# Optimization experiments

Hardware: AMD Instinct MI355X
Metric: run time of the kernel (lower is better)

The kernel has to match this reference:

```python
import jax, jax.numpy as jnp
import numpy as np

N_TRANSFORMS = 24
N_INIT = 5
SOFT_BLEND = 5.0
MAX_STEPS = 8   # reduced from 50 for reference runtime; same per-step math
CVG = 1e-5
DVG = 1.0
EPS = 1e-6


def posi_enc(x):
    # min_deg=0, max_deg=4, append_identity: [...,3] -> [...,27]
    scales = jnp.asarray([1.0, 2.0, 4.0, 8.0], x.dtype)
    xb = (x[..., None, :] * scales[:, None]).reshape(x.shape[:-1] + (12,))
    return jnp.concatenate([x, jnp.sin(xb), jnp.cos(xb)], axis=-1)


def mlp(h, params):
    for W, b in params[:-1]:
        h = jax.nn.relu(h @ W + b)
    W, b = params[-1]
    return h @ W + b


def setup_inputs() -> dict:
    key = jax.random.key(0)
    ks = jax.random.split(key, 16)
    B, N, J = 1, 32768, N_TRANSFORMS
    x = jax.random.normal(ks[0], (B, N, 3), jnp.float32)
    bone_pts = jax.random.normal(ks[1], (J, 3), jnp.float32)

    def near_id(k):
        A = jnp.eye(4, dtype=jnp.float32) + 0.05 * jax.random.normal(k, (J, 4, 4), jnp.float32)
        return A.at[:, 3, :].set(jnp.asarray([0.0, 0.0, 0.0, 1.0], jnp.float32))

    inp = dict(
        x=x, bone_pts=bone_pts,
        transforms=near_id(ks[2]), delta_transforms=near_id(ks[3]),
        W0=0.1 * jax.random.normal(ks[4], (27, 128), jnp.float32), b0=jnp.zeros((128,), jnp.float32),
        W1=0.1 * jax.random.normal(ks[5], (128, 128), jnp.float32), b1=jnp.zeros((128,), jnp.float32),
        W2=0.1 * jax.random.normal(ks[6], (128, 128), jnp.float32), b2=jnp.zeros((128,), jnp.float32),
        W3=0.1 * jax.random.normal(ks[7], (128, 128), jnp.float32), b3=jnp.zeros((128,), jnp.float32),
        W4=0.1 * jax.random.normal(ks[8], (128, 25), jnp.float32), b4=jnp.zeros((25,), jnp.float32),
    )
    return inp


def reference(x, bone_pts, transforms, delta_transforms, W0, b0, W1, b1, W2, b2, W3, b3, W4, b4):
    params = [(W0, b0), (W1, b1), (W2, b2), (W3, b3), (W4, b4)]
    B, N, _ = x.shape
    I = N_INIT + 1  # with_bkgd appends identity init
    dt = x.dtype

    # ---- _initialize_canonical: KNN over bone distances, gather delta transforms
    d = jnp.linalg.norm(x[:, :, None, :] - bone_pts, axis=-1)          # [B,N,J]
    idx = jax.lax.top_k(-d, N_INIT)[1]                                  # [B,N,5]
    Tsel = delta_transforms[idx]                                        # [B,N,5,4,4]
    eye4 = jnp.broadcast_to(jnp.eye(4, dtype=dt), (B, N, 1, 4, 4))
    Tinit = jnp.concatenate([Tsel, eye4], axis=2)                       # [B,N,I,4,4]
    xh = jnp.concatenate([x, jnp.ones_like(x[..., :1])], axis=-1)
    xc0 = jnp.einsum('bnipq,bnq->bnip', Tinit[..., :3, :4], xh)         # [B,N,I,3]

    M = B * N * I
    target = jnp.broadcast_to(x[:, :, None, :], (B, N, I, 3)).reshape(M, 3)
    x0 = xc0.reshape(M, 3)
    Tfull = jnp.concatenate([transforms, jnp.eye(4, dtype=dt)[None]], axis=0)  # [J+1,4,4]

    def g(xc):  # forward-skinning residual g(x_cano) = LBS(x_cano) - x_world
        w = jax.nn.softmax(SOFT_BLEND * mlp(posi_enc(xc), params), axis=-1)   # [M,25]
        tf = jnp.einsum('mj,jpq->mpq', w, Tfull)                               # [M,4,4]
        return jnp.einsum('mpq,mq->mp', tf[:, :3, :3], xc) + tf[:, :3, 3] - target

    # ---- Broyden with dense per-point masking (replaces torch boolean indexing)
    Jinv0 = jnp.broadcast_to(jnp.eye(3, dtype=dt), (M, 3, 3))
    gx0 = g(x0)
    upd0 = -(Jinv0 @ gx0[:, :, None])[:, :, 0]
    norm0 = jnp.linalg.norm(gx0, axis=-1)
    zeros3 = jnp.zeros((M, 3), dt)
    state = (x0, gx0, Jinv0, upd0, x0, norm0, zeros3, zeros3, jnp.ones((M,), bool))

    def body(_, s):
        xk, gx, Jinv, upd, xopt, nopt, dx, dgx, mask = s
        m3 = mask[:, None]
        dx = jnp.where(m3, upd, dx)
        xk = jnp.where(m3, xk + dx, xk)
        gnew = g(xk)
        dgx = jnp.where(m3, gnew - gx, dgx)
        gx = jnp.where(m3, gx + dgx, gx)
        gn = jnp.linalg.norm(gx, axis=-1)
        better = gn < nopt
        nopt = jnp.where(better, gn, nopt)
        xopt = jnp.where(better[:, None], xk, xopt)
        mask = (nopt > CVG) & (gn < DVG)
        vT = dx[:, None, :] @ Jinv                                      # [M,1,3]
        a = dx[:, :, None] - Jinv @ dgx[:, :, None]                      # [M,3,1]
        b = vT @ dgx[:, :, None]                                         # [M,1,1]
        b = b + jnp.where(b >= 0, EPS, -EPS)
        Jinv = jnp.where(mask[:, None, None], Jinv + (a / b) @ vT, Jinv)
        upd = jnp.where(m3, -(Jinv @ gx[:, :, None])[:, :, 0], upd)
        return (xk, gx, Jinv, upd, xopt, nopt, dx, dgx, mask)

    state = jax.lax.fori_loop(0, MAX_STEPS, body, state)
    xopt, nopt = state[4], state[5]
    xopt = jax.lax.stop_gradient(xopt)  # torch detaches the root solve
    valid = nopt < CVG

    # differentiable final forward skinning at the found canonical points
    w = jax.nn.softmax(SOFT_BLEND * mlp(posi_enc(xopt), params), axis=-1)
    tf = jnp.einsum('mj,jpq->mpq', w, Tfull)
    xw = jnp.einsum('mpq,mq->mp', tf[:, :3, :3], xopt) + tf[:, :3, 3]

    return (xw.reshape(B, N, I, 3), xopt.reshape(B, N, I, 3),
            nopt.reshape(B, N, I), valid.reshape(B, N, I))
```

## Files before the change

### kernel.cpp

```cpp
#include <hip/hip_runtime.h>
#include <math.h>

#define BLOCK 256
#define PPB 64
#define HP 132
#define WCOLS 2136
#define NTILES 56

typedef float v2f __attribute__((ext_vector_type(2)));

__device__ __forceinline__ v2f mkv2(float a, float b) {
    v2f r; r.x = a; r.y = b; return r;
}
__device__ __forceinline__ v2f pkfma(v2f a, v2f b, v2f c) {
#if __has_builtin(__builtin_elementwise_fma)
    return __builtin_elementwise_fma(a, b, c);
#else
    return mkv2(fmaf(a.x, b.x, c.x), fmaf(a.y, b.y, c.y));
#endif
}
__device__ __forceinline__ float f4el(const float4& v, int r) {
    return (r == 0) ? v.x : (r == 1) ? v.y : (r == 2) ? v.z : v.w;
}
__device__ __forceinline__ int col_base(int p) { return p * HP + ((p >> 2) << 3); }

__global__ void prep_kernel(const float* __restrict__ W0, const float* __restrict__ W1,
                            const float* __restrict__ W2, const float* __restrict__ W3,
                            const float* __restrict__ W4, const float* __restrict__ b4,
                            float* __restrict__ Wt, float* __restrict__ b4p) {
    const int d = blockIdx.x * blockDim.x + threadIdx.x;
    if (d < NTILES * 1024) {
        const int t = d >> 10, w = d & 1023;
        float v;
        if (t < 52) {
            const int r = w >> 7, rem = w & 127;
            const int half = rem >> 6, q = (rem >> 2) & 15, jl = rem & 3;
            const int col = q * 8 + half * 4 + jl;
            if (t < 4)       { const int k = t * 8 + r;        v = (k < 27) ? W0[k * 128 + col] : 0.f; }
            else if (t < 20) { const int k = (t - 4) * 8 + r;  v = W1[k * 128 + col]; }
            else if (t < 36) { const int k = (t - 20) * 8 + r; v = W2[k * 128 + col]; }
            else             { const int k = (t - 36) * 8 + r; v = W3[k * 128 + col]; }
        } else {
            const int r = w >> 5, rem = w & 31;
            const int half = (rem >> 4) & 1, s = (rem >> 2) & 3, jl = rem & 3;
            const int col = s * 8 + half * 4 + jl;
            const int k = (t - 52) * 32 + r;
            v = (col < 25) ? W4[k * 25 + col] : 0.f;
        }
        Wt[d] = v;
    }
    if (d < 32) b4p[d] = (d < 25) ? b4[d] : 0.f;
}

__device__ __forceinline__ void batch4(const float* wt, int r0, int cg,
                                       const float* hg, int k0,
                                       v2f* __restrict__ acc) {
    float4 h4[4];
#pragma unroll
    for (int p = 0; p < 4; ++p) h4[p] = *(const float4*)(hg + p * HP + k0);
    float4 w0[4], w1[4];
#pragma unroll
    for (int r = 0; r < 4; ++r) {
        w0[r] = *(const float4*)(wt + (r0 + r) * 128 + cg * 4);
        w1[r] = *(const float4*)(wt + (r0 + r) * 128 + 64 + cg * 4);
    }
#pragma unroll
    for (int r = 0; r < 4; ++r) {
        const v2f wa = mkv2(w0[r].x, w0[r].y), wb2 = mkv2(w0[r].z, w0[r].w);
        const v2f wc = mkv2(w1[r].x, w1[r].y), wd = mkv2(w1[r].z, w1[r].w);
#pragma unroll
        for (int p = 0; p < 4; ++p) {
            const float hv = f4el(h4[p], r);
            const v2f hh = mkv2(hv, hv);
            acc[p * 4 + 0] = pkfma(hh, wa, acc[p * 4 + 0]);
            acc[p * 4 + 1] = pkfma(hh, wb2, acc[p * 4 + 1]);
            acc[p * 4 + 2] = pkfma(hh, wc, acc[p * 4 + 2]);
            acc[p * 4 + 3] = pkfma(hh, wd, acc[p * 4 + 3]);
        }
    }
}

__global__ __launch_bounds__(BLOCK)
__attribute__((amdgpu_num_vgpr(128))) void snarf_kernel(
    const float* __restrict__ xin, const float* __restrict__ bone_pts,
    const float* __restrict__ transforms, const float* __restrict__ delta_tf,
    const float* __restrict__ Wt, const float* __restrict__ b0,
    const float* __restrict__ b1, const float* __restrict__ b2,
    const float* __restrict__ b3, const float* __restrict__ b4p,
    float* __restrict__ out, int Npts) {
    __shared__ float hL[4 * WCOLS];
    __shared__ float stL[25 * PPB];
    __shared__ float wb[2][1024];
    __shared__ int flags[4];
    const int tid = threadIdx.x;
    const int wid = tid >> 6;
    const int lane = tid & 63;
    const int p16 = lane & 15;
    const int sq = lane >> 4;
    const int cg = lane >> 2;
    const int gg = lane & 3;
    const int M = Npts * 6;
    const int m = blockIdx.x * PPB + wid * 16 + p16;
    const int mc = (m < M) ? m : (M - 1);
    const int n = mc / 6;
    const int i = mc - n * 6;

    float* hWv = &hL[wid * WCOLS];
    const float* hg = hWv + gg * 536;
    float* hwr = hWv + gg * 536 + 8 * cg;
    float* hq = hWv + col_base(p16);
    volatile float* st = &stL[wid * 16 + p16];
#define STS(idx) st[(idx) * PPB]

    const float tx = xin[n * 3 + 0], ty = xin[n * 3 + 1], tz = xin[n * 3 + 2];

    float xk0, xk1, xk2;
    if (i < 5) {
        float dprev = -1.0f;
        int jprev = -1;
        for (int r = 0; r <= i; ++r) {
            float bd = 3.4028235e38f;
            int bj = 0;
            for (int j = 0; j < 24; ++j) {
                const float ax = tx - bone_pts[j * 3 + 0];
                const float ay = ty - bone_pts[j * 3 + 1];
                const float az = tz - bone_pts[j * 3 + 2];
                const float d = sqrtf(ax * ax + ay * ay + az * az);
                const bool taken = (d < dprev) || (d == dprev && j <= jprev);
                if (!taken && d < bd) { bd = d; bj = j; }
            }
            dprev = bd;
            jprev = bj;
        }
        const float* T = delta_tf + jprev * 16;
        xk0 = fmaf(T[0], tx, fmaf(T[1], ty, fmaf(T[2], tz, T[3])));
        xk1 = fmaf(T[4], tx, fmaf(T[5], ty, fmaf(T[6], tz, T[7])));
        xk2 = fmaf(T[8], tx, fmaf(T[9], ty, fmaf(T[10], tz, T[11])));
    } else {
        xk0 = tx; xk1 = ty; xk2 = tz;
    }

    float gx0 = 0.f, gx1 = 0.f, gx2 = 0.f;
    bool mask = (m < M);

    int cur = 0;
    *(float4*)(&wb[0][0] + tid * 4) = *(const float4*)(Wt + tid * 4);
    __syncthreads();

    for (int step = -1; step < 8; ++step) {
        bool m3 = mask;
        if (step >= 0) {
            __syncthreads();
            if ((flags[0] | flags[1] | flags[2] | flags[3]) == 0) break;
            if (m3) {
                const float u0 = STS(9), u1 = STS(10), u2 = STS(11);
                STS(12) = u0; STS(13) = u1; STS(14) = u2;
                xk0 += u0; xk1 += u1; xk2 += u2;
            }
        }
        const float cx0 = xk0, cx1 = xk1, cx2 = xk2;

        {
            const float f = (float)(1 << sq);
            float sx, cxv, sy, cyv, sz, czv;
            sincosf(f * cx0, &sx, &cxv);
            sincosf(f * cx1, &sy, &cyv);
            sincosf(f * cx2, &sz, &czv);
            if (sq == 0) { hq[0] = cx0; hq[1] = cx1; hq[2] = cx2; }
            const int sb = 3 + sq * 3;
            hq[sb + 0] = sx;  hq[sb + 1] = sy;  hq[sb + 2] = sz;
            hq[sb + 12] = cxv; hq[sb + 13] = cyv; hq[sb + 14] = czv;
            if (sq == 3) {
                hq[27] = 0.f; hq[28] = 0.f; hq[29] = 0.f; hq[30] = 0.f; hq[31] = 0.f;
            }
        }

        __builtin_amdgcn_s_setprio(1);
#pragma unroll 1
        for (int L = 0; L < 4; ++L) {
            const int tbase = (L == 0) ? 0 : (4 + (L - 1) * 16);
            const int NT = (L == 0) ? 4 : 16;
            const float* bc = ((L == 0) ? b0 : (L == 1) ? b1 : (L == 2) ? b2 : b3) + 8 * cg;
            v2f acc[16];
            {
                const float4 b0v = *(const float4*)(bc);
                const float4 b1v = *(const float4*)(bc + 4);
#pragma unroll
                for (int p = 0; p < 4; ++p) {
                    acc[p * 4 + 0] = mkv2(b0v.x, b0v.y);
                    acc[p * 4 + 1] = mkv2(b0v.z, b0v.w);
                    acc[p * 4 + 2] = mkv2(b1v.x, b1v.y);
                    acc[p * 4 + 3] = mkv2(b1v.z, b1v.w);
                }
            }
#pragma unroll 1
            for (int t = 0; t < NT; ++t) {
                const float4 stg = *(const float4*)(Wt + (tbase + t + 1) * 1024 + tid * 4);
                batch4(&wb[cur][0], 0, cg, hg, t * 8, acc);
                batch4(&wb[cur][0], 4, cg, hg, t * 8 + 4, acc);
                *(float4*)(&wb[cur ^ 1][0] + tid * 4) = stg;
                __syncthreads();
                cur ^= 1;
            }
#pragma unroll
            for (int p = 0; p < 4; ++p) {
                float4 o0, o1;
                o0.x = fmaxf(acc[p * 4 + 0].x, 0.f); o0.y = fmaxf(acc[p * 4 + 0].y, 0.f);
                o0.z = fmaxf(acc[p * 4 + 1].x, 0.f); o0.w = fmaxf(acc[p * 4 + 1].y, 0.f);
                o1.x = fmaxf(acc[p * 4 + 2].x, 0.f); o1.y = fmaxf(acc[p * 4 + 2].y, 0.f);
                o1.z = fmaxf(acc[p * 4 + 3].x, 0.f); o1.w = fmaxf(acc[p * 4 + 3].y, 0.f);
                *(float4*)(hwr + p * HP) = o0;
                *(float4*)(hwr + p * HP + 4) = o1;
            }
        }

        {
            v2f la[4];
            const float4 bb0 = *(const float4*)(b4p + 8 * sq);
            const float4 bb1 = *(const float4*)(b4p + 8 * sq + 4);
            la[0] = mkv2(bb0.x, bb0.y); la[1] = mkv2(bb0.z, bb0.w);
            la[2] = mkv2(bb1.x, bb1.y); la[3] = mkv2(bb1.z, bb1.w);
#pragma unroll 1
            for (int t = 0; t < 4; ++t) {
                const int nt = (t < 3) ? (53 + t) : 0;
                const float4 stg = *(const float4*)(Wt + nt * 1024 + tid * 4);
                const float* wt = &wb[cur][0];
#pragma unroll 2
                for (int kb = 0; kb < 8; ++kb) {
                    const float4 h4 = *(const float4*)(hq + t * 32 + kb * 4);
#pragma unroll
                    for (int r = 0; r < 4; ++r) {
                        const float4 w0 = *(const float4*)(wt + (kb * 4 + r) * 32 + sq * 4);
                        const float4 w1 = *(const float4*)(wt + (kb * 4 + r) * 32 + 16 + sq * 4);
                        const float hv = f4el(h4, r);
                        const v2f hh = mkv2(hv, hv);
                        la[0] = pkfma(hh, mkv2(w0.x, w0.y), la[0]);
                        la[1] = pkfma(hh, mkv2(w0.z, w0.w), la[1]);
                        la[2] = pkfma(hh, mkv2(w1.x, w1.y), la[2]);
                        la[3] = pkfma(hh, mkv2(w1.z, w1.w), la[3]);
                    }
                }
                *(float4*)(&wb[cur ^ 1][0] + tid * 4) = stg;
                __syncthreads();
                cur ^= 1;
            }
            __builtin_amdgcn_s_setprio(0);
            float4 o0, o1;
            o0.x = la[0].x; o0.y = la[0].y; o0.z = la[1].x; o0.w = la[1].y;
            o1.x = la[2].x; o1.y = la[2].y; o1.z = la[3].x; o1.w = la[3].y;
            *(float4*)(hq + 8 * sq) = o0;
            *(float4*)(hq + 8 * sq + 4) = o1;
        }

        float l25[25];
        {
            const float4 r0 = *(const float4*)(hq + 0);
            const float4 r1 = *(const float4*)(hq + 4);
            const float4 r2 = *(const float4*)(hq + 8);
            const float4 r3 = *(const float4*)(hq + 12);
            const float4 r4 = *(const float4*)(hq + 16);
            const float4 r5 = *(const float4*)(hq + 20);
            l25[0] = r0.x; l25[1] = r0.y; l25[2] = r0.z; l25[3] = r0.w;
            l25[4] = r1.x; l25[5] = r1.y; l25[6] = r1.z; l25[7] = r1.w;
            l25[8] = r2.x; l25[9] = r2.y; l25[10] = r2.z; l25[11] = r2.w;
            l25[12] = r3.x; l25[13] = r3.y; l25[14] = r3.z; l25[15] = r3.w;
            l25[16] = r4.x; l25[17] = r4.y; l25[18] = r4.z; l25[19] = r4.w;
            l25[20] = r5.x; l25[21] = r5.y; l25[22] = r5.z; l25[23] = r5.w;
            l25[24] = hq[24];
        }

        float zm = -3.4028235e38f;
#pragma unroll
        for (int j = 0; j < 25; ++j) {
            l25[j] = 5.0f * l25[j];
            zm = fmaxf(zm, l25[j]);
        }
        float ssum = 0.f;
#pragma unroll
        for (int j = 0; j < 25; ++j) {
            l25[j] = expf(l25[j] - zm);
            ssum += l25[j];
        }
        const float inv = 1.0f / ssum;

        float tf[12];
#pragma unroll
        for (int r = 0; r < 12; ++r) tf[r] = 0.f;
#pragma unroll
        for (int j = 0; j < 24; ++j) {
            const float wj = l25[j] * inv;
            const float* T = transforms + j * 16;
#pragma unroll
            for (int r = 0; r < 12; ++r) tf[r] = fmaf(wj, T[r], tf[r]);
        }
        {
            const float wj = l25[24] * inv;
            tf[0] += wj; tf[5] += wj; tf[10] += wj;
        }
        const float r0 = fmaf(tf[0], cx0, fmaf(tf[1], cx1, fmaf(tf[2], cx2, tf[3])));
        const float r1 = fmaf(tf[4], cx0, fmaf(tf[5], cx1, fmaf(tf[6], cx2, tf[7])));
        const float r2 = fmaf(tf[8], cx0, fmaf(tf[9], cx1, fmaf(tf[10], cx2, tf[11])));

        const float g0 = r0 - tx, g1 = r1 - ty, g2 = r2 - tz;

        if (step == -1) {
            gx0 = g0; gx1 = g1; gx2 = g2;
            const float gn = sqrtf(g0 * g0 + g1 * g1 + g2 * g2);
            STS(21) = gn;
            STS(9) = -g0; STS(10) = -g1; STS(11) = -g2;
            STS(18) = xk0; STS(19) = xk1; STS(20) = xk2;
            STS(22) = r0; STS(23) = r1; STS(24) = r2;
            STS(12) = 0.f; STS(13) = 0.f; STS(14) = 0.f;
            STS(15) = 0.f; STS(16) = 0.f; STS(17) = 0.f;
            STS(0) = 1.f; STS(1) = 0.f; STS(2) = 0.f;
            STS(3) = 0.f; STS(4) = 1.f; STS(5) = 0.f;
            STS(6) = 0.f; STS(7) = 0.f; STS(8) = 1.f;
        } else {
            float J00 = STS(0), J01 = STS(1), J02 = STS(2);
            float J10 = STS(3), J11 = STS(4), J12 = STS(5);
            float J20 = STS(6), J21 = STS(7), J22 = STS(8);
            const float dx0 = STS(12), dx1 = STS(13), dx2 = STS(14);
            float dg0 = STS(15), dg1 = STS(16), dg2 = STS(17);
            float nopt = STS(21);
            if (m3) {
                dg0 = g0 - gx0; dg1 = g1 - gx1; dg2 = g2 - gx2;
                gx0 += dg0; gx1 += dg1; gx2 += dg2;
                STS(15) = dg0; STS(16) = dg1; STS(17) = dg2;
            }
            const float gn = sqrtf(gx0 * gx0 + gx1 * gx1 + gx2 * gx2);
            const bool better = gn < nopt;
            if (better) {
                nopt = gn;
                STS(21) = gn;
                STS(18) = xk0; STS(19) = xk1; STS(20) = xk2;
                STS(22) = r0; STS(23) = r1; STS(24) = r2;
            }
            mask = (nopt > 1e-5f) && (gn < 1.0f) && (m < M);

            const float v0 = dx0 * J00 + dx1 * J10 + dx2 * J20;
            const float v1 = dx0 * J01 + dx1 * J11 + dx2 * J21;
            const float v2 = dx0 * J02 + dx1 * J12 + dx2 * J22;
            const float Jd0 = J00 * dg0 + J01 * dg1 + J02 * dg2;
            const float Jd1 = J10 * dg0 + J11 * dg1 + J12 * dg2;
            const float Jd2 = J20 * dg0 + J21 * dg1 + J22 * dg2;
            const float a0 = dx0 - Jd0, a1 = dx1 - Jd1, a2 = dx2 - Jd2;
            float bden = v0 * dg0 + v1 * dg1 + v2 * dg2;
            bden += (bden >= 0.f) ? 1e-6f : -1e-6f;
            if (mask) {
                const float q0 = a0 / bden, q1 = a1 / bden, q2 = a2 / bden;
                J00 = fmaf(q0, v0, J00); J01 = fmaf(q0, v1, J01); J02 = fmaf(q0, v2, J02);
                J10 = fmaf(q1, v0, J10); J11 = fmaf(q1, v1, J11); J12 = fmaf(q1, v2, J12);
                J20 = fmaf(q2, v0, J20); J21 = fmaf(q2, v1, J21); J22 = fmaf(q2, v2, J22);
                STS(0) = J00; STS(1) = J01; STS(2) = J02;
                STS(3) = J10; STS(4) = J11; STS(5) = J12;
                STS(6) = J20; STS(7) = J21; STS(8) = J22;
            }
            if (m3) {
                STS(9) = -(J00 * gx0 + J01 * gx1 + J02 * gx2);
                STS(10) = -(J10 * gx0 + J11 * gx1 + J12 * gx2);
                STS(11) = -(J20 * gx0 + J21 * gx1 + J22 * gx2);
            }
        }
        {
            const unsigned long long b = __ballot(mask);
            if (lane == 0) flags[wid] = (b != 0ull) ? 1 : 0;
        }
    }

    if (sq == 0 && m < M) {
        const float nopt = STS(21);
        out[(size_t)m * 3 + 0] = STS(22);
        out[(size_t)m * 3 + 1] = STS(23);
        out[(size_t)m * 3 + 2] = STS(24);
        float* xopt_out = out + (size_t)M * 3;
        xopt_out[(size_t)m * 3 + 0] = STS(18);
        xopt_out[(size_t)m * 3 + 1] = STS(19);
        xopt_out[(size_t)m * 3 + 2] = STS(20);
        out[(size_t)M * 6 + m] = nopt;
        out[(size_t)M * 7 + m] = (nopt < 1e-5f) ? 1.0f : 0.0f;
    }
#undef STS
}

extern "C" void kernel_launch(void* const* d_in, const int* in_sizes, int n_in,
                              void* d_out, int out_size, void* d_ws, size_t ws_size,
                              hipStream_t stream) {
    const float* x = (const float*)d_in[0];
    const float* bone_pts = (const float*)d_in[1];
    const float* transforms = (const float*)d_in[2];
    const float* delta_tf = (const float*)d_in[3];
    const float* W0 = (const float*)d_in[4];
    const float* b0 = (const float*)d_in[5];
    const float* W1 = (const float*)d_in[6];
    const float* b1 = (const float*)d_in[7];
    const float* W2 = (const float*)d_in[8];
    const float* b2 = (const float*)d_in[9];
    const float* W3 = (const float*)d_in[10];
    const float* b3 = (const float*)d_in[11];
    const float* W4 = (const float*)d_in[12];
    const float* b4 = (const float*)d_in[13];
    float* out = (float*)d_out;

    float* Wt = (float*)d_ws;
    float* b4p = Wt + NTILES * 1024;

    prep_kernel<<<(NTILES * 1024 + 255) / 256, 256, 0, stream>>>(
        W0, W1, W2, W3, W4, b4, Wt, b4p);

    const int Npts = in_sizes[0] / 3;
    const int M = Npts * 6;
    const int blocks = (M + PPB - 1) / PPB;
    snarf_kernel<<<blocks, BLOCK, 0, stream>>>(
        x, bone_pts, transforms, delta_tf, Wt, b0, b1, b2, b3, b4p, out, Npts);
}
```

Before: 1.747 ms.

## Use single-wave blocks with async global-to-LDS weight staging and no block barriers

Blocks shrink from four waves covering 64 points to one wave covering 32 points. Each lane now accumulates an 8-point by 8-column tile, which doubles the reuse of each weight read from LDS. Weight tiles are double-buffered with global_load_lds and a vmcnt wait instead of register staging plus __syncthreads, and the convergence check becomes a wave ballot. The intent is to remove block-wide barriers and register round-trips for weight staging. The cost is a larger accumulator register footprint under the 128-VGPR cap and a different LDS and occupancy balance.

```diff
diff --git a/kernel.cpp b/kernel.cpp
--- a/kernel.cpp
+++ b/kernel.cpp
@@ -1,10 +1,9 @@
 #include <hip/hip_runtime.h>
 #include <math.h>
-
-#define BLOCK 256
-#define PPB 64
-#define HP 132
-#define WCOLS 2136
+#include <stdint.h>
+
+#define BLOCK 64
+#define PPW 32
 #define NTILES 56
 
 typedef float v2f __attribute__((ext_vector_type(2)));
@@ -22,7 +21,26 @@
 __device__ __forceinline__ float f4el(const float4& v, int r) {
     return (r == 0) ? v.x : (r == 1) ? v.y : (r == 2) ? v.z : v.w;
 }
-__device__ __forceinline__ int col_base(int p) { return p * HP + ((p >> 2) << 3); }
+
+#define VMWAIT() asm volatile("s_waitcnt vmcnt(0)" ::: "memory")
+
+__device__ __forceinline__ void stage_tile(const float* __restrict__ Wt, int t,
+                                           float* dst, int lane) {
+    const float* src = Wt + t * 1024 + lane * 4;
+    float* d0 = dst + lane * 4;
+    __builtin_amdgcn_global_load_lds(
+        (const __attribute__((address_space(1))) uint32_t*)src,
+        (__attribute__((address_space(3))) uint32_t*)d0, 16, 0, 0);
+    __builtin_amdgcn_global_load_lds(
+        (const __attribute__((address_space(1))) uint32_t*)(src + 256),
+        (__attribute__((address_space(3))) uint32_t*)(d0 + 256), 16, 0, 0);
+    __builtin_amdgcn_global_load_lds(
+        (const __attribute__((address_space(1))) uint32_t*)(src + 512),
+        (__attribute__((address_space(3))) uint32_t*)(d0 + 512), 16, 0, 0);
+    __builtin_amdgcn_global_load_lds(
+        (const __attribute__((address_space(1))) uint32_t*)(src + 768),
+        (__attribute__((address_space(3))) uint32_t*)(d0 + 768), 16, 0, 0);
+}
 
 __global__ void prep_kernel(const float* __restrict__ W0, const float* __restrict__ W1,
                             const float* __restrict__ W2, const float* __restrict__ W3,
@@ -41,42 +59,82 @@
             else if (t < 36) { const int k = (t - 20) * 8 + r; v = W2[k * 128 + col]; }
             else             { const int k = (t - 36) * 8 + r; v = W3[k * 128 + col]; }
         } else {
-            const int r = w >> 5, rem = w & 31;
-            const int half = (rem >> 4) & 1, s = (rem >> 2) & 3, jl = rem & 3;
-            const int col = s * 8 + half * 4 + jl;
+            const int r = w >> 5, c = w & 31;
             const int k = (t - 52) * 32 + r;
-            v = (col < 25) ? W4[k * 25 + col] : 0.f;
+            v = (c < 25) ? W4[k * 25 + c] : 0.f;
         }
         Wt[d] = v;
     }
     if (d < 32) b4p[d] = (d < 25) ? b4[d] : 0.f;
 }
 
-__device__ __forceinline__ void batch4(const float* wt, int r0, int cg,
-                                       const float* hg, int k0,
+__device__ __forceinline__ void batch2(const float* wt, int kt, int cg,
+                                       const float* hgg, int kh,
                                        v2f* __restrict__ acc) {
-    float4 h4[4];
-#pragma unroll
-    for (int p = 0; p < 4; ++p) h4[p] = *(const float4*)(hg + p * HP + k0);
-    float4 w0[4], w1[4];
-#pragma unroll
-    for (int r = 0; r < 4; ++r) {
-        w0[r] = *(const float4*)(wt + (r0 + r) * 128 + cg * 4);
-        w1[r] = *(const float4*)(wt + (r0 + r) * 128 + 64 + cg * 4);
-    }
-#pragma unroll
-    for (int r = 0; r < 4; ++r) {
-        const v2f wa = mkv2(w0[r].x, w0[r].y), wb2 = mkv2(w0[r].z, w0[r].w);
-        const v2f wc = mkv2(w1[r].x, w1[r].y), wd = mkv2(w1[r].z, w1[r].w);
-#pragma unroll
-        for (int p = 0; p < 4; ++p) {
-            const float hv = f4el(h4[p], r);
-            const v2f hh = mkv2(hv, hv);
-            acc[p * 4 + 0] = pkfma(hh, wa, acc[p * 4 + 0]);
-            acc[p * 4 + 1] = pkfma(hh, wb2, acc[p * 4 + 1]);
-            acc[p * 4 + 2] = pkfma(hh, wc, acc[p * 4 + 2]);
-            acc[p * 4 + 3] = pkfma(hh, wd, acc[p * 4 + 3]);
-        }
+    const float4 w00 = *(const float4*)(wt + kt * 128 + cg * 4);
+    const float4 w01 = *(const float4*)(wt + kt * 128 + 64 + cg * 4);
+    const float4 w10 = *(const float4*)(wt + (kt + 1) * 128 + cg * 4);
+    const float4 w11 = *(const float4*)(wt + (kt + 1) * 128 + 64 + cg * 4);
+    v2f h[8];
+#pragma unroll
+    for (int j = 0; j < 8; ++j) h[j] = *(const v2f*)(hgg + j * 132 + kh);
+    const v2f a0 = mkv2(w00.x, w00.y), a1 = mkv2(w00.z, w00.w);
+    const v2f a2 = mkv2(w01.x, w01.y), a3 = mkv2(w01.z, w01.w);
+    const v2f b0v = mkv2(w10.x, w10.y), b1v = mkv2(w10.z, w10.w);
+    const v2f b2v = mkv2(w11.x, w11.y), b3v = mkv2(w11.z, w11.w);
+#pragma unroll
+    for (int j = 0; j < 8; ++j) {
+        v2f hh = mkv2(h[j].x, h[j].x);
+        acc[j * 4 + 0] = pkfma(hh, a0, acc[j * 4 + 0]);
+        acc[j * 4 + 1] = pkfma(hh, a1, acc[j * 4 + 1]);
+        acc[j * 4 + 2] = pkfma(hh, a2, acc[j * 4 + 2]);
+        acc[j * 4 + 3] = pkfma(hh, a3, acc[j * 4 + 3]);
+        hh = mkv2(h[j].y, h[j].y);
+        acc[j * 4 + 0] = pkfma(hh, b0v, acc[j * 4 + 0]);
+        acc[j * 4 + 1] = pkfma(hh, b1v, acc[j * 4 + 1]);
+        acc[j * 4 + 2] = pkfma(hh, b2v, acc[j * 4 + 2]);
+        acc[j * 4 + 3] = pkfma(hh, b3v, acc[j * 4 + 3]);
+    }
+}
+
+template <int NT>
+__device__ __forceinline__ void main_layer(const float* __restrict__ Wt,
+                                           const float* __restrict__ bL,
+                                           float (*wb)[1024], int& cur, int& gt,
+                                           const float* hgg, float* hwr,
+                                           int cg, int lane) {
+    v2f acc[32];
+    {
+        const float4 bb0 = *(const float4*)(bL + 8 * cg);
+        const float4 bb1 = *(const float4*)(bL + 8 * cg + 4);
+#pragma unroll
+        for (int j = 0; j < 8; ++j) {
+            acc[j * 4 + 0] = mkv2(bb0.x, bb0.y);
+            acc[j * 4 + 1] = mkv2(bb0.z, bb0.w);
+            acc[j * 4 + 2] = mkv2(bb1.x, bb1.y);
+            acc[j * 4 + 3] = mkv2(bb1.z, bb1.w);
+        }
+    }
+#pragma unroll 1
+    for (int t = 0; t < NT; ++t) {
+        VMWAIT();
+        stage_tile(Wt, (gt == 55) ? 0 : (gt + 1), &wb[cur ^ 1][0], lane);
+        const float* wt = &wb[cur][0];
+#pragma unroll
+        for (int b = 0; b < 4; ++b)
+            batch2(wt, b * 2, cg, hgg, t * 8 + b * 2, acc);
+        cur ^= 1;
+        ++gt;
+    }
+#pragma unroll
+    for (int j = 0; j < 8; ++j) {
+        float4 o0, o1;
+        o0.x = fmaxf(acc[j * 4 + 0].x, 0.f); o0.y = fmaxf(acc[j * 4 + 0].y, 0.f);
+        o0.z = fmaxf(acc[j * 4 + 1].x, 0.f); o0.w = fmaxf(acc[j * 4 + 1].y, 0.f);
+        o1.x = fmaxf(acc[j * 4 + 2].x, 0.f); o1.y = fmaxf(acc[j * 4 + 2].y, 0.f);
+        o1.z = fmaxf(acc[j * 4 + 3].x, 0.f); o1.w = fmaxf(acc[j * 4 + 3].y, 0.f);
+        *(float4*)(hwr + j * 132) = o0;
+        *(float4*)(hwr + j * 132 + 4) = o1;
     }
 }
 
@@ -88,29 +146,28 @@
     const float* __restrict__ b1, const float* __restrict__ b2,
     const float* __restrict__ b3, const float* __restrict__ b4p,
     float* __restrict__ out, int Npts) {
-    __shared__ float hL[4 * WCOLS];
-    __shared__ float stL[25 * PPB];
+    __shared__ float hL[4248];
+    __shared__ float stL[25 * PPW];
     __shared__ float wb[2][1024];
-    __shared__ int flags[4];
-    const int tid = threadIdx.x;
-    const int wid = tid >> 6;
-    const int lane = tid & 63;
-    const int p16 = lane & 15;
-    const int sq = lane >> 4;
+    const int lane = threadIdx.x;
     const int cg = lane >> 2;
     const int gg = lane & 3;
+    const int p32 = lane & 31;
+    const int du = lane >> 5;
     const int M = Npts * 6;
-    const int m = blockIdx.x * PPB + wid * 16 + p16;
+    const int m = blockIdx.x * PPW + p32;
     const int mc = (m < M) ? m : (M - 1);
     const int n = mc / 6;
     const int i = mc - n * 6;
 
-    float* hWv = &hL[wid * WCOLS];
-    const float* hg = hWv + gg * 536;
-    float* hwr = hWv + gg * 536 + 8 * cg;
-    float* hq = hWv + col_base(p16);
-    volatile float* st = &stL[wid * 16 + p16];
-#define STS(idx) st[(idx) * PPB]
+    float* hq = hL + p32 * 132 + ((p32 >> 3) << 3);
+    const float* hgg = hL + gg * 1064;
+    float* hwr = hL + gg * 1064 + 8 * cg;
+    volatile float* st = &stL[p32];
+#define STS(idx) st[(idx) * PPW]
+
+    stage_tile(Wt, 0, &wb[0][0], lane);
+    int cur = 0;
 
     const float tx = xin[n * 3 + 0], ty = xin[n * 3 + 1], tz = xin[n * 3 + 2];
 
@@ -143,15 +200,10 @@
     float gx0 = 0.f, gx1 = 0.f, gx2 = 0.f;
     bool mask = (m < M);
 
-    int cur = 0;
-    *(float4*)(&wb[0][0] + tid * 4) = *(const float4*)(Wt + tid * 4);
-    __syncthreads();
-
     for (int step = -1; step < 8; ++step) {
         bool m3 = mask;
         if (step >= 0) {
-            __syncthreads();
-            if ((flags[0] | flags[1] | flags[2] | flags[3]) == 0) break;
+            if (__ballot(mask) == 0ull) break;
             if (m3) {
                 const float u0 = STS(9), u1 = STS(10), u2 = STS(11);
                 STS(12) = u0; STS(13) = u1; STS(14) = u2;
@@ -161,95 +213,86 @@
         const float cx0 = xk0, cx1 = xk1, cx2 = xk2;
 
         {
-            const float f = (float)(1 << sq);
-            float sx, cxv, sy, cyv, sz, czv;
-            sincosf(f * cx0, &sx, &cxv);
-            sincosf(f * cx1, &sy, &cyv);
-            sincosf(f * cx2, &sz, &czv);
-            if (sq == 0) { hq[0] = cx0; hq[1] = cx1; hq[2] = cx2; }
-            const int sb = 3 + sq * 3;
-            hq[sb + 0] = sx;  hq[sb + 1] = sy;  hq[sb + 2] = sz;
-            hq[sb + 12] = cxv; hq[sb + 13] = cyv; hq[sb + 14] = czv;
-            if (sq == 3) {
+            const float fa = du ? 4.f : 1.f;
+            float sax, cax, say, cay, saz, caz;
+            float sbx, cbx, sby, cby, sbz, cbz;
+            sincosf(fa * cx0, &sax, &cax);
+            sincosf(fa * cx1, &say, &cay);
+            sincosf(fa * cx2, &saz, &caz);
+            sincosf(2.f * fa * cx0, &sbx, &cbx);
+            sincosf(2.f * fa * cx1, &sby, &cby);
+            sincosf(2.f * fa * cx2, &sbz, &cbz);
+            const int sa = 3 + du * 6;
+            hq[sa + 0] = sax; hq[sa + 1] = say; hq[sa + 2] = saz;
+            hq[sa + 3] = sbx; hq[sa + 4] = sby; hq[sa + 5] = sbz;
+            hq[sa + 12] = cax; hq[sa + 13] = cay; hq[sa + 14] = caz;
+            hq[sa + 15] = cbx; hq[sa + 16] = cby; hq[sa + 17] = cbz;
+            if (du == 0) {
+                hq[0] = cx0; hq[1] = cx1; hq[2] = cx2;
+            } else {
                 hq[27] = 0.f; hq[28] = 0.f; hq[29] = 0.f; hq[30] = 0.f; hq[31] = 0.f;
             }
         }
 
         __builtin_amdgcn_s_setprio(1);
-#pragma unroll 1
-        for (int L = 0; L < 4; ++L) {
-            const int tbase = (L == 0) ? 0 : (4 + (L - 1) * 16);
-            const int NT = (L == 0) ? 4 : 16;
-            const float* bc = ((L == 0) ? b0 : (L == 1) ? b1 : (L == 2) ? b2 : b3) + 8 * cg;
-            v2f acc[16];
+        int gt = 0;
+        main_layer<4>(Wt, b0, wb, cur, gt, hgg, hwr, cg, lane);
+        main_layer<16>(Wt, b1, wb, cur, gt, hgg, hwr, cg, lane);
+        main_layer<16>(Wt, b2, wb, cur, gt, hgg, hwr, cg, lane);
+        main_layer<16>(Wt, b3, wb, cur, gt, hgg, hwr, cg, lane);
+
+        {
+            v2f la[8];
             {
-                const float4 b0v = *(const float4*)(bc);
-                const float4 b1v = *(const float4*)(bc + 4);
-#pragma unroll
-                for (int p = 0; p < 4; ++p) {
-                    acc[p * 4 + 0] = mkv2(b0v.x, b0v.y);
-                    acc[p * 4 + 1] = mkv2(b0v.z, b0v.w);
-                    acc[p * 4 + 2] = mkv2(b1v.x, b1v.y);
-                    acc[p * 4 + 3] = mkv2(b1v.z, b1v.w);
-                }
-            }
-#pragma unroll 1
-            for (int t = 0; t < NT; ++t) {
-                const float4 stg = *(const float4*)(Wt + (tbase + t + 1) * 1024 + tid * 4);
-                batch4(&wb[cur][0], 0, cg, hg, t * 8, acc);
-                batch4(&wb[cur][0], 4, cg, hg, t * 8 + 4, acc);
-                *(float4*)(&wb[cur ^ 1][0] + tid * 4) = stg;
-                __syncthreads();
-                cur ^= 1;
-            }
-#pragma unroll
-            for (int p = 0; p < 4; ++p) {
-                float4 o0, o1;
-                o0.x = fmaxf(acc[p * 4 + 0].x, 0.f); o0.y = fmaxf(acc[p * 4 + 0].y, 0.f);
-                o0.z = fmaxf(acc[p * 4 + 1].x, 0.f); o0.w = fmaxf(acc[p * 4 + 1].y, 0.f);
-                o1.x = fmaxf(acc[p * 4 + 2].x, 0.f); o1.y = fmaxf(acc[p * 4 + 2].y, 0.f);
-                o1.z = fmaxf(acc[p * 4 + 3].x, 0.f); o1.w = fmaxf(acc[p * 4 + 3].y, 0.f);
-                *(float4*)(hwr + p * HP) = o0;
-                *(float4*)(hwr + p * HP + 4) = o1;
-            }
-        }
-
-        {
-            v2f la[4];
-            const float4 bb0 = *(const float4*)(b4p + 8 * sq);
-            const float4 bb1 = *(const float4*)(b4p + 8 * sq + 4);
-            la[0] = mkv2(bb0.x, bb0.y); la[1] = mkv2(bb0.z, bb0.w);
-            la[2] = mkv2(bb1.x, bb1.y); la[3] = mkv2(bb1.z, bb1.w);
+                const float* bc = b4p + du * 16;
+                const float4 bb0 = *(const float4*)(bc);
+                const float4 bb1 = *(const float4*)(bc + 4);
+                const float4 bb2 = *(const float4*)(bc + 8);
+                const float4 bb3 = *(const float4*)(bc + 12);
+                la[0] = mkv2(bb0.x, bb0.y); la[1] = mkv2(bb0.z, bb0.w);
+                la[2] = mkv2(bb1.x, bb1.y); la[3] = mkv2(bb1.z, bb1.w);
+                la[4] = mkv2(bb2.x, bb2.y); la[5] = mkv2(bb2.z, bb2.w);
+                la[6] = mkv2(bb3.x, bb3.y); la[7] = mkv2(bb3.z, bb3.w);
+            }
 #pragma unroll 1
             for (int t = 0; t < 4; ++t) {
-                const int nt = (t < 3) ? (53 + t) : 0;
-                const float4 stg = *(const float4*)(Wt + nt * 1024 + tid * 4);
+                VMWAIT();
+                stage_tile(Wt, (t < 3) ? (53 + t) : 0, &wb[cur ^ 1][0], lane);
                 const float* wt = &wb[cur][0];
 #pragma unroll 2
                 for (int kb = 0; kb < 8; ++kb) {
                     const float4 h4 = *(const float4*)(hq + t * 32 + kb * 4);
 #pragma unroll
                     for (int r = 0; r < 4; ++r) {
-                        const float4 w0 = *(const float4*)(wt + (kb * 4 + r) * 32 + sq * 4);
-                        const float4 w1 = *(const float4*)(wt + (kb * 4 + r) * 32 + 16 + sq * 4);
+                        const float* wr = wt + (kb * 4 + r) * 32 + du * 16;
+                        const float4 w0 = *(const float4*)(wr);
+                        const float4 w1 = *(const float4*)(wr + 4);
+                        const float4 w2 = *(const float4*)(wr + 8);
+                        const float4 w3 = *(const float4*)(wr + 12);
                         const float hv = f4el(h4, r);
                         const v2f hh = mkv2(hv, hv);
                         la[0] = pkfma(hh, mkv2(w0.x, w0.y), la[0]);
                         la[1] = pkfma(hh, mkv2(w0.z, w0.w), la[1]);
                         la[2] = pkfma(hh, mkv2(w1.x, w1.y), la[2]);
                         la[3] = pkfma(hh, mkv2(w1.z, w1.w), la[3]);
+                        la[4] = pkfma(hh, mkv2(w2.x, w2.y), la[4]);
+                        la[5] = pkfma(hh, mkv2(w2.z, w2.w), la[5]);
+                        la[6] = pkfma(hh, mkv2(w3.x, w3.y), la[6]);
+                        la[7] = pkfma(hh, mkv2(w3.z, w3.w), la[7]);
                     }
                 }
-                *(float4*)(&wb[cur ^ 1][0] + tid * 4) = stg;
-                __syncthreads();
                 cur ^= 1;
             }
             __builtin_amdgcn_s_setprio(0);
-            float4 o0, o1;
+            float4 o0, o1, o2, o3;
             o0.x = la[0].x; o0.y = la[0].y; o0.z = la[1].x; o0.w = la[1].y;
             o1.x = la[2].x; o1.y = la[2].y; o1.z = la[3].x; o1.w = la[3].y;
-            *(float4*)(hq + 8 * sq) = o0;
-            *(float4*)(hq + 8 * sq + 4) = o1;
+            o2.x = la[4].x; o2.y = la[4].y; o2.z = la[5].x; o2.w = la[5].y;
+            o3.x = la[6].x; o3.y = la[6].y; o3.z = la[7].x; o3.w = la[7].y;
+            *(float4*)(hq + du * 16 + 0) = o0;
+            *(float4*)(hq + du * 16 + 4) = o1;
+            *(float4*)(hq + du * 16 + 8) = o2;
+            *(float4*)(hq + du * 16 + 12) = o3;
         }
 
         float l25[25];
@@ -361,13 +404,9 @@
                 STS(11) = -(J20 * gx0 + J21 * gx1 + J22 * gx2);
             }
         }
-        {
-            const unsigned long long b = __ballot(mask);
-            if (lane == 0) flags[wid] = (b != 0ull) ? 1 : 0;
-        }
-    }
-
-    if (sq == 0 && m < M) {
+    }
+
+    if (du == 0 && m < M) {
         const float nopt = STS(21);
         out[(size_t)m * 3 + 0] = STS(22);
         out[(size_t)m * 3 + 1] = STS(23);
@@ -409,7 +448,7 @@
 
     const int Npts = in_sizes[0] / 3;
     const int M = Npts * 6;
-    const int blocks = (M + PPB - 1) / PPB;
+    const int blocks = (M + PPW - 1) / PPW;
     snarf_kernel<<<blocks, BLOCK, 0, stream>>>(
         x, bone_pts, transforms, delta_tf, Wt, b0, b1, b2, b3, b4p, out, Npts);
 }
```

After: 1.965 ms. 12.5% more time.

## Triple-buffer weight tiles with direct global-to-LDS async loads

Applied to the files above, without the earlier changes.

Replaces the register-staged double-buffered weight tile copy with a three-stage ring that loads global memory straight into LDS via global_load_lds. Each tile iteration waits on vmcnt(1) and then a barrier before issuing the load two tiles ahead, so the fetch overlaps the FMA work and the VGPR round trip plus trailing syncthreads are gone. It costs another 4 KB of LDS, and correctness rests on the hand-written waitcnt/barrier ordering and the tile-index wraparound across steps.

```diff
diff --git a/kernel.cpp b/kernel.cpp
--- a/kernel.cpp
+++ b/kernel.cpp
@@ -1,5 +1,6 @@
 #include <hip/hip_runtime.h>
 #include <math.h>
+#include <stdint.h>
 
 #define BLOCK 256
 #define PPB 64
@@ -23,6 +24,13 @@
     return (r == 0) ? v.x : (r == 1) ? v.y : (r == 2) ? v.z : v.w;
 }
 __device__ __forceinline__ int col_base(int p) { return p * HP + ((p >> 2) << 3); }
+
+__device__ __forceinline__ void stage1(const float* __restrict__ Wt, int t,
+                                       float* dst, int tid) {
+    __builtin_amdgcn_global_load_lds(
+        (const __attribute__((address_space(1))) uint32_t*)(Wt + t * 1024 + tid * 4),
+        (__attribute__((address_space(3))) uint32_t*)(dst + tid * 4), 16, 0, 0);
+}
 
 __global__ void prep_kernel(const float* __restrict__ W0, const float* __restrict__ W1,
                             const float* __restrict__ W2, const float* __restrict__ W3,
@@ -80,6 +88,13 @@
     }
 }
 
+#define TILE_SYNC()                                          \
+    do {                                                     \
+        asm volatile("s_waitcnt vmcnt(1)" ::: "memory");     \
+        __builtin_amdgcn_s_barrier();                        \
+        __builtin_amdgcn_sched_barrier(0);                   \
+    } while (0)
+
 __global__ __launch_bounds__(BLOCK)
 __attribute__((amdgpu_num_vgpr(128))) void snarf_kernel(
     const float* __restrict__ xin, const float* __restrict__ bone_pts,
@@ -90,7 +105,7 @@
     float* __restrict__ out, int Npts) {
     __shared__ float hL[4 * WCOLS];
     __shared__ float stL[25 * PPB];
-    __shared__ float wb[2][1024];
+    __shared__ float wb[3][1024];
     __shared__ int flags[4];
     const int tid = threadIdx.x;
     const int wid = tid >> 6;
@@ -111,6 +126,10 @@
     float* hq = hWv + col_base(p16);
     volatile float* st = &stL[wid * 16 + p16];
 #define STS(idx) st[(idx) * PPB]
+
+    stage1(Wt, 0, &wb[0][0], tid);
+    stage1(Wt, 1, &wb[1][0], tid);
+    int cur = 0;
 
     const float tx = xin[n * 3 + 0], ty = xin[n * 3 + 1], tz = xin[n * 3 + 2];
 
@@ -143,10 +162,6 @@
     float gx0 = 0.f, gx1 = 0.f, gx2 = 0.f;
     bool mask = (m < M);
 
-    int cur = 0;
-    *(float4*)(&wb[0][0] + tid * 4) = *(const float4*)(Wt + tid * 4);
-    __syncthreads();
-
     for (int step = -1; step < 8; ++step) {
         bool m3 = mask;
         if (step >= 0) {
@@ -176,9 +191,9 @@
         }
 
         __builtin_amdgcn_s_setprio(1);
+        int gt = 0;
 #pragma unroll 1
         for (int L = 0; L < 4; ++L) {
-            const int tbase = (L == 0) ? 0 : (4 + (L - 1) * 16);
             const int NT = (L == 0) ? 4 : 16;
             const float* bc = ((L == 0) ? b0 : (L == 1) ? b1 : (L == 2) ? b2 : b3) + 8 * cg;
             v2f acc[16];
@@ -195,12 +210,16 @@
             }
 #pragma unroll 1
             for (int t = 0; t < NT; ++t) {
-                const float4 stg = *(const float4*)(Wt + (tbase + t + 1) * 1024 + tid * 4);
+                TILE_SYNC();
+                {
+                    const int nst = gt + 2;
+                    const int cur2 = (cur >= 1) ? (cur - 1) : 2;
+                    stage1(Wt, (nst >= NTILES) ? (nst - NTILES) : nst, &wb[cur2][0], tid);
+                }
                 batch4(&wb[cur][0], 0, cg, hg, t * 8, acc);
                 batch4(&wb[cur][0], 4, cg, hg, t * 8 + 4, acc);
-                *(float4*)(&wb[cur ^ 1][0] + tid * 4) = stg;
-                __syncthreads();
-                cur ^= 1;
+                cur = (cur == 2) ? 0 : (cur + 1);
+                ++gt;
             }
 #pragma unroll
             for (int p = 0; p < 4; ++p) {
@@ -222,8 +241,12 @@
             la[2] = mkv2(bb1.x, bb1.y); la[3] = mkv2(bb1.z, bb1.w);
 #pragma unroll 1
             for (int t = 0; t < 4; ++t) {
-                const int nt = (t < 3) ? (53 + t) : 0;
-                const float4 stg = *(const float4*)(Wt + nt * 1024 + tid * 4);
+                TILE_SYNC();
+                {
+                    const int nst = gt + 2;
+                    const int cur2 = (cur >= 1) ? (cur - 1) : 2;
+                    stage1(Wt, (nst >= NTILES) ? (nst - NTILES) : nst, &wb[cur2][0], tid);
+                }
                 const float* wt = &wb[cur][0];
 #pragma unroll 2
                 for (int kb = 0; kb < 8; ++kb) {
@@ -240,9 +263,8 @@
                         la[3] = pkfma(hh, mkv2(w1.z, w1.w), la[3]);
                     }
                 }
-                *(float4*)(&wb[cur ^ 1][0] + tid * 4) = stg;
-                __syncthreads();
-                cur ^= 1;
+                cur = (cur == 2) ? 0 : (cur + 1);
+                ++gt;
             }
             __builtin_amdgcn_s_setprio(0);
             float4 o0, o1;
```

Result: no change. 1.778 ms (+1.8%).
